# Kernel optimization log

Hardware: AMD Instinct MI355X
Metric: run time of the kernel (lower is better)

## Reference

```python
import jax, jax.numpy as jnp
import numpy as np

N, D, P = 4096, 1024, 2048
TAU, ALPHA = 0.2, 0.8
GAMMA_EX, GAMMA_IN = 2.0, 1.6
EPS = 1e-8


def _cos_sim(e):
    # F.cosine_similarity(e[:,None], e[None,:], dim=2) == normalized rows matmul
    n = jnp.linalg.norm(e, axis=1, keepdims=True)
    en = e / jnp.maximum(n, EPS)
    return en @ en.T  # [N, N]


def setup_inputs() -> dict:
    key = jax.random.key(0)
    embeddings = jax.random.normal(key, (N, D), dtype=jnp.float32)
    # positive pairs: (0,1),(2,3),... (arange fill)
    pp = np.arange(2 * P).reshape(P, 2)
    pos_partner = np.arange(N)
    pos_partner[pp[:, 0]] = pp[:, 1]
    pos_partner[pp[:, 1]] = pp[:, 0]
    # negative pairs = all ordered (i,j), i!=j, minus ordered positive tuples,
    # enumerated row-major (deterministic stand-in for torch's set order).
    pos_m = np.zeros((N, N), dtype=bool)
    pos_m[pp[:, 0], pp[:, 1]] = True
    neg_m = ~np.eye(N, dtype=bool) & ~pos_m
    ii, jj = np.nonzero(neg_m)  # row-major order
    neg_partner = np.arange(N)
    neg_partner[ii] = jj
    neg_partner[jj] = ii  # processed[j] = ... overwrites after
    return {
        "embeddings": embeddings,
        "positive_pairs": jnp.asarray(pp, jnp.int32),
        "pos_partner": jnp.asarray(pos_partner, jnp.int32),
        "neg_partner": jnp.asarray(neg_partner, jnp.int32),
    }


def reference(embeddings, positive_pairs, pos_partner, neg_partner):
    pi, pj = positive_pairs[:, 0], positive_pairs[:, 1]
    # Beta(gamma,gamma) scalar mixing coefficients (dim_mixing=False)
    lam_pos = jax.random.beta(jax.random.key(1), GAMMA_EX, GAMMA_EX) + 1.0  # 'ex'
    lam_neg = jax.random.beta(jax.random.key(2), GAMMA_IN, GAMMA_IN)        # 'in'

    orig = _cos_sim(embeddings)
    hp = _cos_sim(lam_pos * embeddings + (1.0 - lam_pos) * embeddings[pos_partner])
    hn = _cos_sim(lam_neg * embeddings + (1.0 - lam_neg) * embeddings[neg_partner])

    eye = jnp.eye(N, dtype=bool)
    pos_m = jnp.zeros((N, N), dtype=bool).at[pi, pj].set(True)  # ordered positives
    neg_m = ~eye & ~pos_m                                        # ordered negatives
    # pos replacement first, then neg replacement overwrites (faithful ordering)
    sim = jnp.where(pos_m | pos_m.T, hp, orig)
    sim = jnp.where(neg_m | neg_m.T, hn, sim)

    # ----- compute_loss (stage='train': quantile hard-negative mining) -----
    mask = eye | pos_m | pos_m.T
    exp_sim = jnp.exp(sim / TAU)
    exp_masked = jnp.where(mask, 0.0, exp_sim)
    pos_ij = exp_sim[pi, pj]
    pos_ji = exp_sim[pj, pi]
    exp_i = exp_masked[pi]  # [P, N]
    exp_j = exp_masked[pj]
    thr_i = jnp.quantile(exp_i, ALPHA, axis=1, keepdims=True)
    thr_j = jnp.quantile(exp_j, ALPHA, axis=1, keepdims=True)
    sum_i = jnp.where(exp_i >= thr_i, exp_i, 0.0).sum(axis=1)
    sum_j = jnp.where(exp_j >= thr_j, exp_j, 0.0).sum(axis=1)
    loss_ij = -jnp.log(pos_ij / (pos_ij + sum_i))
    loss_ji = -jnp.log(pos_ji / (pos_ji + sum_j))
    return (loss_ij + loss_ji).sum() / (2 * P)
```

## Files before the change

### kernel.cpp

```cpp
#include <hip/hip_runtime.h>
#include <hip/hip_bf16.h>

#define NN 4096
#define DD 1024
constexpr float LAM = 0.45f;
constexpr float INV_TAU = 5.0f;
constexpr int KSEL = 820;
constexpr unsigned KEY_BASE = 0x3B80u;
constexpr int NBINS = 2048;

typedef __attribute__((ext_vector_type(8))) short bf16x8;
typedef __attribute__((ext_vector_type(4))) float f32x4;

__device__ inline void async_copy16(const ushort* g, ushort* l) {
    __builtin_amdgcn_global_load_lds(
        (const __attribute__((address_space(1))) void*)g,
        (__attribute__((address_space(3))) void*)l, 16, 0, 0);
}

__global__ __launch_bounds__(256) void mixnorm_kernel(const float* __restrict__ E,
                                                      const int* __restrict__ negp,
                                                      ushort* __restrict__ U) {
    int r = blockIdx.x, t = threadIdx.x;
    int p = negp[r];
    const float a = LAM, b = 1.0f - LAM;
    float4 x = ((const float4*)(E + (size_t)r * DD))[t];
    float4 y = ((const float4*)(E + (size_t)p * DD))[t];
    float4 m;
    m.x = a * x.x + b * y.x;
    m.y = a * x.y + b * y.y;
    m.z = a * x.z + b * y.z;
    m.w = a * x.w + b * y.w;
    float ss = m.x * m.x + m.y * m.y + m.z * m.z + m.w * m.w;
    #pragma unroll
    for (int off = 32; off > 0; off >>= 1) ss += __shfl_down(ss, off, 64);
    __shared__ float part[4];
    if ((t & 63) == 0) part[t >> 6] = ss;
    __syncthreads();
    float tot = part[0] + part[1] + part[2] + part[3];
    float inv = 1.0f / fmaxf(sqrtf(tot), 1e-8f);
    ushort4 o;
    o.x = __bfloat16_as_ushort(__float2bfloat16(m.x * inv));
    o.y = __bfloat16_as_ushort(__float2bfloat16(m.y * inv));
    o.z = __bfloat16_as_ushort(__float2bfloat16(m.z * inv));
    o.w = __bfloat16_as_ushort(__float2bfloat16(m.w * inv));
    ((ushort4*)(U + (size_t)r * DD))[t] = o;
}

__global__ __launch_bounds__(512) void gemm_exp_kernel(const ushort* __restrict__ U,
                                                       ushort* __restrict__ Z) {
    __shared__ ushort sm_all[16384];
    ushort* A = sm_all;
    ushort* B = sm_all + 8192;
    const int t = threadIdx.x;
    const int w = t >> 6, l = t & 63;

    const int m = blockIdx.x;
    float fdec = sqrtf(8.0f * (float)m + 1.0f);
    int by = (int)((fdec - 1.0f) * 0.5f);
    while ((by + 1) * (by + 2) / 2 <= m) by++;
    while (by * (by + 1) / 2 > m) by--;
    const int bx = m - by * (by + 1) / 2;

    const ushort* gA = U + (size_t)(by * 128 + (t >> 2)) * DD + (t & 3) * 8;
    const ushort* gB = U + (size_t)(bx * 128 + (t >> 2)) * DD + (t & 3) * 8;
    ushort* lA0 = A + w * 512;
    ushort* lA1 = A + 4096 + w * 512;
    ushort* lB0 = B + w * 512;
    ushort* lB1 = B + 4096 + w * 512;

    f32x4 acc[2][4];
    #pragma unroll
    for (int i = 0; i < 2; i++)
        #pragma unroll
        for (int j = 0; j < 4; j++) acc[i][j] = (f32x4){0.f, 0.f, 0.f, 0.f};

    const int wr = w >> 1, wc = w & 1;
    const int mrow = wr * 32 + (l & 15);
    const int nrow = wc * 64 + (l & 15);
    const int kq = (l >> 4) * 8;

    for (int k0 = 0; k0 < DD; k0 += 64) {
        async_copy16(gA, lA0);
        async_copy16(gA + 32, lA1);
        async_copy16(gB, lB0);
        async_copy16(gB + 32, lB1);
        gA += 64; gB += 64;
        __syncthreads();
        #pragma unroll
        for (int kh = 0; kh < 2; kh++) {
            const ushort* Ah = A + kh * 4096;
            const ushort* Bh = B + kh * 4096;
            bf16x8 af[2], bfr[4];
            #pragma unroll
            for (int i = 0; i < 2; i++)
                af[i] = *(const bf16x8*)(Ah + (mrow + i * 16) * 32 + kq);
            #pragma unroll
            for (int j = 0; j < 4; j++)
                bfr[j] = *(const bf16x8*)(Bh + (nrow + j * 16) * 32 + kq);
            #pragma unroll
            for (int i = 0; i < 2; i++)
                #pragma unroll
                for (int j = 0; j < 4; j++)
                    acc[i][j] = __builtin_amdgcn_mfma_f32_16x16x32_bf16(af[i], bfr[j], acc[i][j], 0, 0, 0);
        }
        __syncthreads();
    }

    ushort* smv = sm_all;
    ushort* smT = sm_all + 4096;
    const bool mirror = (bx != by);
    #pragma unroll
    for (int h = 0; h < 4; h++) {
        __syncthreads();
        if (wr == h) {
            #pragma unroll
            for (int i = 0; i < 2; i++)
                #pragma unroll
                for (int j = 0; j < 4; j++)
                    #pragma unroll
                    for (int rg = 0; rg < 4; rg++) {
                        float v = __expf(acc[i][j][rg] * INV_TAU);
                        ushort hv = __bfloat16_as_ushort(__float2bfloat16(v));
                        int lrow = i * 16 + ((l >> 4) << 2) + rg;
                        int lcol = (wc << 6) + j * 16 + (l & 15);
                        smv[lrow * 128 + lcol] = hv;
                        smT[lcol * 48 + lrow] = hv;
                    }
        }
        __syncthreads();
        {
            const uint4* src = (const uint4*)(smv + (t >> 4) * 128 + (t & 15) * 8);
            uint4* dst = (uint4*)(Z + (size_t)(by * 128 + h * 32 + (t >> 4)) * NN + bx * 128 + (t & 15) * 8);
            *dst = *src;
        }
        if (mirror) {
            const uint4* srcT = (const uint4*)(smT + (t >> 2) * 48 + (t & 3) * 8);
            uint4* dstT = (uint4*)(Z + (size_t)(bx * 128 + (t >> 2)) * NN + by * 128 + h * 32 + (t & 3) * 8);
            *dstT = *srcT;
        }
    }
}

__global__ __launch_bounds__(256) void rowloss_kernel(const ushort* __restrict__ Z,
                                                      const int* __restrict__ posp,
                                                      float* __restrict__ loss) {
    __shared__ unsigned histall[4][2][NBINS / 2];
    const int t = threadIdx.x, w = t >> 6, l = t & 63;
    const int r = blockIdx.x * 4 + w;
    unsigned* hist = histall[w][l & 1];
    const int p = posp[r];
    const uint4* zr = (const uint4*)(Z + (size_t)r * NN);

    #pragma unroll
    for (int q = 0; q < 8; q++)
        ((uint4*)histall[w])[l * 8 + q] = (uint4){0u, 0u, 0u, 0u};

    const float posv = __uint_as_float(((unsigned)Z[(size_t)r * NN + p]) << 16);

    #pragma unroll
    for (int c = 0; c < 8; c++) {
        uint4 v = zr[c * 64 + l];
        unsigned wd[4] = {v.x, v.y, v.z, v.w};
        const int cb = (c * 64 + l) * 8;
        #pragma unroll
        for (int q = 0; q < 4; q++) {
            unsigned lo = wd[q] & 0xFFFFu;
            unsigned hi = wd[q] >> 16;
            int c0 = cb + 2 * q, c1 = c0 + 1;
            lo = (c0 == p || c0 == r) ? 0u : lo;
            hi = (c1 == p || c1 == r) ? 0u : hi;
            int b0 = max(0, min(NBINS - 1, (int)lo - (int)KEY_BASE));
            int b1 = max(0, min(NBINS - 1, (int)hi - (int)KEY_BASE));
            atomicAdd(&hist[b0 >> 1], 1u << ((b0 & 1) * 16));
            atomicAdd(&hist[b1 >> 1], 1u << ((b1 & 1) * 16));
        }
    }

    unsigned ow[16];
    {
        const uint4* h0 = (const uint4*)(histall[w][0] + l * 16);
        const uint4* h1 = (const uint4*)(histall[w][1] + l * 16);
        #pragma unroll
        for (int q = 0; q < 4; q++) {
            uint4 x0 = h0[q];
            uint4 x1 = h1[q];
            ow[4 * q]     = x0.x + x1.x;
            ow[4 * q + 1] = x0.y + x1.y;
            ow[4 * q + 2] = x0.z + x1.z;
            ow[4 * q + 3] = x0.w + x1.w;
        }
    }
    unsigned lsum = 0;
    #pragma unroll
    for (int i = 0; i < 16; i++) lsum += (ow[i] & 0xFFFFu) + (ow[i] >> 16);
    unsigned S = lsum;
    #pragma unroll
    for (int d = 1; d < 64; d <<= 1) {
        unsigned o = __shfl_down(S, d, 64);
        if (l + d < 64) S += o;
    }
    const bool cross = (S >= (unsigned)KSEL) && (S - lsum) < (unsigned)KSEL;
    int bstar = 0;
    if (cross) {
        int rem = KSEL - (int)(S - lsum);
        int a2 = 0;
        #pragma unroll
        for (int i = 31; i >= 0; i--) {
            unsigned c = (ow[i >> 1] >> ((i & 1) * 16)) & 0xFFFFu;
            a2 += (int)c;
            if (a2 >= rem) { bstar = l * 32 + i; break; }
        }
    }
    unsigned long long bm = __ballot(cross);
    int src = __ffsll((long long)bm) - 1;
    bstar = __shfl(bstar, src, 64);

    float s = 0.f;
    #pragma unroll
    for (int i = 0; i < 32; i++) {
        int g = l * 32 + i;
        unsigned c = (ow[i >> 1] >> ((i & 1) * 16)) & 0xFFFFu;
        if (g >= bstar && c) {
            float val = __uint_as_float((KEY_BASE + (unsigned)g) << 16);
            s = fmaf((float)c, val, s);
        }
    }
    #pragma unroll
    for (int off = 32; off > 0; off >>= 1) s += __shfl_down(s, off, 64);
    if (l == 0) loss[r] = log1pf(s / posv);
}

__global__ __launch_bounds__(256) void finalize_kernel(const float* __restrict__ loss,
                                                       unsigned* __restrict__ out) {
    __shared__ float part[4];
    const int t = threadIdx.x, w = t >> 6, l = t & 63;
    float s = 0.f;
    #pragma unroll
    for (int q = 0; q < 4; q++) {
        float4 v = ((const float4*)loss)[t * 4 + q];
        s += (v.x + v.y) + (v.z + v.w);
    }
    #pragma unroll
    for (int off = 32; off > 0; off >>= 1) s += __shfl_down(s, off, 64);
    if (l == 0) part[w] = s;
    __syncthreads();
    if (t == 0) {
        float v = (part[0] + part[1] + part[2] + part[3]) * (1.0f / 4096.0f);
        unsigned short bits = __bfloat16_as_ushort(__float2bfloat16(v));
        *out = ((unsigned)bits << 16) | (unsigned)bits;
    }
}

extern "C" void kernel_launch(void* const* d_in, const int* in_sizes, int n_in,
                              void* d_out, int out_size, void* d_ws, size_t ws_size,
                              hipStream_t stream) {
    const float* E = (const float*)d_in[0];
    const int* posp = (const int*)d_in[2];
    const int* negp = (const int*)d_in[3];

    float* loss = (float*)d_ws;
    ushort* U = (ushort*)((char*)d_ws + 16384);
    ushort* Z = (ushort*)((char*)d_ws + 16384 + (size_t)NN * DD * 2);
    
    mixnorm_kernel<<<NN, 256, 0, stream>>>(E, negp, U);
    gemm_exp_kernel<<<528, 512, 0, stream>>>(U, Z);
    rowloss_kernel<<<NN / 4, 256, 0, stream>>>(Z, posp, loss);
    finalize_kernel<<<1, 256, 0, stream>>>(loss, (unsigned*)d_out);
}
```

Measured before the change: 122.7 us.

## Fold final reduction into rowloss via atomics and widen GEMM K-step

Removes the separate finalize kernel launch. Each rowloss block now atomically adds its partial loss into one of 16 accumulators, and the last block to finish (found with an atomic counter) writes the bf16 output. The accumulators are zeroed inside mixnorm_kernel. Separately, the GEMM loads 128-wide K slices per barrier instead of 64, which doubles LDS use to 64KB and halves the number of syncs. Risks are lower occupancy from the larger LDS footprint, and float atomic summation order making the result non-deterministic.

```diff
diff --git a/kernel.cpp b/kernel.cpp
--- a/kernel.cpp
+++ b/kernel.cpp
@@ -8,6 +8,7 @@
 constexpr int KSEL = 820;
 constexpr unsigned KEY_BASE = 0x3B80u;
 constexpr int NBINS = 2048;
+constexpr int NACC = 16;
 
 typedef __attribute__((ext_vector_type(8))) short bf16x8;
 typedef __attribute__((ext_vector_type(4))) float f32x4;
@@ -20,8 +21,14 @@
 
 __global__ __launch_bounds__(256) void mixnorm_kernel(const float* __restrict__ E,
                                                       const int* __restrict__ negp,
-                                                      ushort* __restrict__ U) {
+                                                      ushort* __restrict__ U,
+                                                      float* __restrict__ acc,
+                                                      unsigned* __restrict__ cnt) {
     int r = blockIdx.x, t = threadIdx.x;
+    if (r == 0) {
+        if (t < NACC) acc[t] = 0.0f;
+        if (t == NACC) *cnt = 0u;
+    }
     int p = negp[r];
     const float a = LAM, b = 1.0f - LAM;
     float4 x = ((const float4*)(E + (size_t)r * DD))[t];
@@ -49,9 +56,9 @@
 
 __global__ __launch_bounds__(512) void gemm_exp_kernel(const ushort* __restrict__ U,
                                                        ushort* __restrict__ Z) {
-    __shared__ ushort sm_all[16384];
+    __shared__ ushort sm_all[32768];
     ushort* A = sm_all;
-    ushort* B = sm_all + 8192;
+    ushort* B = sm_all + 16384;
     const int t = threadIdx.x;
     const int w = t >> 6, l = t & 63;
 
@@ -64,10 +71,8 @@
 
     const ushort* gA = U + (size_t)(by * 128 + (t >> 2)) * DD + (t & 3) * 8;
     const ushort* gB = U + (size_t)(bx * 128 + (t >> 2)) * DD + (t & 3) * 8;
-    ushort* lA0 = A + w * 512;
-    ushort* lA1 = A + 4096 + w * 512;
-    ushort* lB0 = B + w * 512;
-    ushort* lB1 = B + 4096 + w * 512;
+    ushort* lA = A + w * 512;
+    ushort* lB = B + w * 512;
 
     f32x4 acc[2][4];
     #pragma unroll
@@ -80,15 +85,16 @@
     const int nrow = wc * 64 + (l & 15);
     const int kq = (l >> 4) * 8;
 
-    for (int k0 = 0; k0 < DD; k0 += 64) {
-        async_copy16(gA, lA0);
-        async_copy16(gA + 32, lA1);
-        async_copy16(gB, lB0);
-        async_copy16(gB + 32, lB1);
-        gA += 64; gB += 64;
-        __syncthreads();
-        #pragma unroll
-        for (int kh = 0; kh < 2; kh++) {
+    for (int k0 = 0; k0 < DD; k0 += 128) {
+        #pragma unroll
+        for (int h = 0; h < 4; h++) {
+            async_copy16(gA + h * 32, lA + h * 4096);
+            async_copy16(gB + h * 32, lB + h * 4096);
+        }
+        gA += 128; gB += 128;
+        __syncthreads();
+        #pragma unroll
+        for (int kh = 0; kh < 4; kh++) {
             const ushort* Ah = A + kh * 4096;
             const ushort* Bh = B + kh * 4096;
             bf16x8 af[2], bfr[4];
@@ -144,8 +150,11 @@
 
 __global__ __launch_bounds__(256) void rowloss_kernel(const ushort* __restrict__ Z,
                                                       const int* __restrict__ posp,
-                                                      float* __restrict__ loss) {
+                                                      float* __restrict__ acc,
+                                                      unsigned* __restrict__ cnt,
+                                                      unsigned* __restrict__ out) {
     __shared__ unsigned histall[4][2][NBINS / 2];
+    __shared__ float lpart[4];
     const int t = threadIdx.x, w = t >> 6, l = t & 63;
     const int r = blockIdx.x * 4 + w;
     unsigned* hist = histall[w][l & 1];
@@ -228,27 +237,22 @@
     }
     #pragma unroll
     for (int off = 32; off > 0; off >>= 1) s += __shfl_down(s, off, 64);
-    if (l == 0) loss[r] = log1pf(s / posv);
-}
-
-__global__ __launch_bounds__(256) void finalize_kernel(const float* __restrict__ loss,
-                                                       unsigned* __restrict__ out) {
-    __shared__ float part[4];
-    const int t = threadIdx.x, w = t >> 6, l = t & 63;
-    float s = 0.f;
-    #pragma unroll
-    for (int q = 0; q < 4; q++) {
-        float4 v = ((const float4*)loss)[t * 4 + q];
-        s += (v.x + v.y) + (v.z + v.w);
-    }
-    #pragma unroll
-    for (int off = 32; off > 0; off >>= 1) s += __shfl_down(s, off, 64);
-    if (l == 0) part[w] = s;
+    if (l == 0) lpart[w] = log1pf(s / posv);
+
     __syncthreads();
     if (t == 0) {
-        float v = (part[0] + part[1] + part[2] + part[3]) * (1.0f / 4096.0f);
-        unsigned short bits = __bfloat16_as_ushort(__float2bfloat16(v));
-        *out = ((unsigned)bits << 16) | (unsigned)bits;
+        float bs = lpart[0] + lpart[1] + lpart[2] + lpart[3];
+        atomicAdd(&acc[blockIdx.x & (NACC - 1)], bs);
+        __threadfence();
+        unsigned old = atomicAdd(cnt, 1u);
+        if (old == gridDim.x - 1) {
+            float tot = 0.f;
+            #pragma unroll
+            for (int i = 0; i < NACC; i++) tot += atomicAdd(&acc[i], 0.0f);
+            float v = tot * (1.0f / 4096.0f);
+            unsigned short bits = __bfloat16_as_ushort(__float2bfloat16(v));
+            *out = ((unsigned)bits << 16) | (unsigned)bits;
+        }
     }
 }
 
@@ -259,12 +263,12 @@
     const int* posp = (const int*)d_in[2];
     const int* negp = (const int*)d_in[3];
 
-    float* loss = (float*)d_ws;
+    float* acc = (float*)d_ws;
+    unsigned* cnt = (unsigned*)((char*)d_ws + 64);
     ushort* U = (ushort*)((char*)d_ws + 16384);
     ushort* Z = (ushort*)((char*)d_ws + 16384 + (size_t)NN * DD * 2);
-    
-    mixnorm_kernel<<<NN, 256, 0, stream>>>(E, negp, U);
+
+    mixnorm_kernel<<<NN, 256, 0, stream>>>(E, negp, U, acc, cnt);
     gemm_exp_kernel<<<528, 512, 0, stream>>>(U, Z);
-    rowloss_kernel<<<NN / 4, 256, 0, stream>>>(Z, posp, loss);
-    finalize_kernel<<<1, 256, 0, stream>>>(loss, (unsigned*)d_out);
-}
+    rowloss_kernel<<<NN / 4, 256, 0, stream>>>(Z, posp, acc, cnt, (unsigned*)d_out);
+}
```

Result: slower. 154.5 us (+25.9%).
